# Performance work log

Hardware: AMD Instinct MI355X
Metric: run time of the kernel (lower is better)

Reference implementation:

```python
import jax, jax.numpy as jnp
import numpy as np
from jax import lax

PCR = (-59.9, -59.9, -2.0, 59.9, 59.9, 5.9)
TOPK = 10
THRESHOLD = 0.5
MARGIN = 0.5
EPS = 1e-8  # torch cosine_similarity default eps


def setup_inputs() -> dict:
    key = jax.random.key(0)
    k1, k2, k3, k4, k5 = jax.random.split(key, 5)
    B, C, H, W, N = 4, 64, 512, 512, 30
    loc_features = jax.random.normal(k1, (B, C, H, W), dtype=jnp.float32)
    det_features = jax.random.normal(k2, (B, C, H, W), dtype=jnp.float32)
    # gt boxes: x,y inside point-cloud range; last element is class id (0 == static)
    xy = jax.random.uniform(k3, (B, N, 2), minval=-55.0, maxval=55.0, dtype=jnp.float32)
    rest = jax.random.normal(k4, (B, N, 5), dtype=jnp.float32)
    cls = jax.random.randint(k5, (B, N, 1), 0, 3).astype(jnp.float32)
    gt_boxes = jnp.concatenate([xy, rest, cls], axis=-1)  # [B, N, 8]
    return {"loc_features": loc_features, "det_features": det_features, "gt_boxes": gt_boxes}


def _loss_fwd(loc_features, det_features, gt_boxes):
    B, C, H, W = loc_features.shape
    bw = PCR[3] - PCR[0]
    bh = PCR[4] - PCR[1]

    def per_batch(loc_fm, det_fm, boxes):
        # --- static GT detection features (gather at box centers) ---
        static_mask = boxes[:, -1] == 0  # [N]
        cx = jnp.clip(((boxes[:, 0] - PCR[0]) / bw * W).astype(jnp.int32), 0, W - 1)
        cy = jnp.clip(((boxes[:, 1] - PCR[1]) / bh * H).astype(jnp.int32), 0, H - 1)
        det_feats = det_fm[:, cy, cx].T  # [N, C]

        # --- find_peaks: local-max of L2 intensity, threshold, top-k (stop-grad) ---
        intensity = lax.stop_gradient(jnp.sqrt(jnp.sum(loc_fm * loc_fm, axis=0)))  # [H, W]
        pooled = lax.reduce_window(intensity, -jnp.inf, lax.max, (3, 3), (1, 1), [(1, 1), (1, 1)])
        peak_mask = (intensity == pooled) & (intensity > THRESHOLD)
        masked = jnp.where(peak_mask, intensity, -jnp.inf).reshape(-1)
        vals, idx = lax.top_k(masked, TOPK)  # descending by intensity
        valid_peak = jnp.isfinite(vals)  # handles < TOPK peaks
        py, px = idx // W, idx % W
        peak_feats = loc_fm[:, py, px].T  # [K, C]

        # --- pairwise cosine similarity (torch eps semantics) ---
        dn = det_feats / jnp.maximum(jnp.linalg.norm(det_feats, axis=-1, keepdims=True), EPS)
        pn = peak_feats / jnp.maximum(jnp.linalg.norm(peak_feats, axis=-1, keepdims=True), EPS)
        sim = jnp.einsum('nc,kc->nk', dn, pn)  # [N, K]

        pair_mask = (static_mask[:, None] & valid_peak[None, :]).astype(sim.dtype)
        n_pairs = jnp.sum(pair_mask)
        loss_sum = jnp.sum(jax.nn.relu(sim - MARGIN) * pair_mask)
        return jnp.where(n_pairs > 0, loss_sum / jnp.maximum(n_pairs, 1.0), 0.0)

    losses = jax.vmap(per_batch)(loc_features, det_features, gt_boxes)  # [B]
    return jnp.sum(losses) / B


def reference(loc_features, det_features, gt_boxes):
    return _loss_fwd(loc_features, det_features, gt_boxes)
```

## Files before the change

kernel.cpp:

```cpp
#include <hip/hip_runtime.h>
#include <math.h>

typedef unsigned long long u64;
typedef unsigned int u32;
typedef float f4 __attribute__((ext_vector_type(4)));

#define HH 512
#define WW 512
#define CC 64
#define HWHW (HH * WW)
#define NBOX 30
#define KTOP 10
#define BLKS_PER_B 256
#define CAND_PER_BATCH (BLKS_PER_B * KTOP)

__global__ void k_intensity(const float* __restrict__ loc, float* __restrict__ inten) {
    int t   = threadIdx.x;
    int blk = blockIdx.x;
    int b   = blk >> 7;
    int j   = blk & 127;
    const f4* base = reinterpret_cast<const f4*>(loc + (size_t)b * CC * HWHW);
    int q0 = j * 512 + t;
    int q1 = q0 + 256;

    f4 s0 = {0.f, 0.f, 0.f, 0.f};
    f4 s1 = {0.f, 0.f, 0.f, 0.f};
    #pragma unroll 8
    for (int c = 0; c < CC; ++c) {
        const f4* p = base + (size_t)c * (HWHW / 4);
        f4 v0 = __builtin_nontemporal_load(p + q0);
        f4 v1 = __builtin_nontemporal_load(p + q1);
        s0 += v0 * v0;
        s1 += v1 * v1;
    }
    f4 o0, o1;
    o0[0] = sqrtf(s0[0]); o0[1] = sqrtf(s0[1]); o0[2] = sqrtf(s0[2]); o0[3] = sqrtf(s0[3]);
    o1[0] = sqrtf(s1[0]); o1[1] = sqrtf(s1[1]); o1[2] = sqrtf(s1[2]); o1[3] = sqrtf(s1[3]);
    f4* out = reinterpret_cast<f4*>(inten + (size_t)b * HWHW);
    out[q0] = o0;
    out[q1] = o1;
}

__global__ void k_peakblock(const float* __restrict__ inten, u64* __restrict__ cand) {
    int t    = threadIdx.x;
    int lane = t & 63;
    int blk  = blockIdx.x;
    int b    = blk >> 8;
    int pblk = blk & 255;
    const float* I = inten + (size_t)b * HWHW;
    int pix0 = pblk * 1024 + t * 4;
    int y  = pix0 >> 9;
    int x0 = pix0 & (WW - 1);

    float w00,w01,w02,w03,w04,w05, w10,w11,w12,w13,w14,w15, w20,w21,w22,w23,w24,w25;
    {
        bool r0 = (y - 1) >= 0, r2 = (y + 1) < HH;
        bool c0 = (x0 - 1) >= 0, c5 = (x0 + 4) < WW;
        const float* Rm = I + (y - 1) * WW + x0;
        const float* Rc = I + y * WW + x0;
        const float* Rp = I + (y + 1) * WW + x0;
        w00 = (r0 && c0) ? Rm[-1] : -INFINITY;
        w01 = r0 ? Rm[0] : -INFINITY;  w02 = r0 ? Rm[1] : -INFINITY;
        w03 = r0 ? Rm[2] : -INFINITY;  w04 = r0 ? Rm[3] : -INFINITY;
        w05 = (r0 && c5) ? Rm[4] : -INFINITY;
        w10 = c0 ? Rc[-1] : -INFINITY;
        w11 = Rc[0]; w12 = Rc[1]; w13 = Rc[2]; w14 = Rc[3];
        w15 = c5 ? Rc[4] : -INFINITY;
        w20 = (r2 && c0) ? Rp[-1] : -INFINITY;
        w21 = r2 ? Rp[0] : -INFINITY;  w22 = r2 ? Rp[1] : -INFINITY;
        w23 = r2 ? Rp[2] : -INFINITY;  w24 = r2 ? Rp[3] : -INFINITY;
        w25 = (r2 && c5) ? Rp[4] : -INFINITY;
    }

    u64 k0, k1, k2, k3;
    {
        float m, v;
        v = w11;
        m = fmaxf(fmaxf(fmaxf(w00, w01), fmaxf(w02, w10)),
                  fmaxf(fmaxf(w11, w12), fmaxf(fmaxf(w20, w21), w22)));
        k0 = (v > 0.5f && v == m) ? (((u64)(__float_as_uint(v) | 0x80000000u) << 32) | (u32)(~(u32)(pix0 + 0))) : 0ull;
        v = w12;
        m = fmaxf(fmaxf(fmaxf(w01, w02), fmaxf(w03, w11)),
                  fmaxf(fmaxf(w12, w13), fmaxf(fmaxf(w21, w22), w23)));
        k1 = (v > 0.5f && v == m) ? (((u64)(__float_as_uint(v) | 0x80000000u) << 32) | (u32)(~(u32)(pix0 + 1))) : 0ull;
        v = w13;
        m = fmaxf(fmaxf(fmaxf(w02, w03), fmaxf(w04, w12)),
                  fmaxf(fmaxf(w13, w14), fmaxf(fmaxf(w22, w23), w24)));
        k2 = (v > 0.5f && v == m) ? (((u64)(__float_as_uint(v) | 0x80000000u) << 32) | (u32)(~(u32)(pix0 + 2))) : 0ull;
        v = w14;
        m = fmaxf(fmaxf(fmaxf(w03, w04), fmaxf(w05, w13)),
                  fmaxf(fmaxf(w14, w15), fmaxf(fmaxf(w23, w24), w25)));
        k3 = (v > 0.5f && v == m) ? (((u64)(__float_as_uint(v) | 0x80000000u) << 32) | (u32)(~(u32)(pix0 + 3))) : 0ull;
    }

    u64 a[4]; int n = 0;
    if (k0) a[n++] = k0;
    if (k1) a[n++] = k1;
    if (k2) a[n++] = k2;
    if (k3) a[n++] = k3;

    __shared__ int cnt;
    __shared__ u64 pool[1024];
    if (t == 0) cnt = 0;
    __syncthreads();

    int incl = n;
    #pragma unroll
    for (int s = 1; s < 64; s <<= 1) {
        int o = __shfl_up(incl, s, 64);
        if (lane >= s) incl += o;
    }
    int excl = incl - n;
    int wtot = __shfl(incl, 63, 64);
    int base = 0;
    if (lane == 0 && wtot > 0) base = atomicAdd(&cnt, wtot);
    base = __shfl(base, 0, 64);
    for (int i = 0; i < n; ++i) pool[base + excl + i] = a[i];
    __syncthreads();

    int total = cnt;
    if (t < 64) {
        u64 lv[KTOP];
        #pragma unroll
        for (int i = 0; i < KTOP; ++i) lv[i] = 0ull;
        for (int j = lane; j < total; j += 64) {
            u64 v = pool[j];
            if (v > lv[KTOP - 1]) {
                lv[KTOP - 1] = v;
                #pragma unroll
                for (int m = KTOP - 1; m > 0; --m)
                    if (lv[m] > lv[m - 1]) { u64 tm = lv[m]; lv[m] = lv[m - 1]; lv[m - 1] = tm; }
            }
        }
        u64 mine = 0;
        #pragma unroll
        for (int r = 0; r < KTOP; ++r) {
            u64 wv = lv[0];
            #pragma unroll
            for (int s = 1; s < 64; s <<= 1) {
                u64 o = __shfl_xor(wv, s, 64);
                wv = (o > wv) ? o : wv;
            }
            if (lane == r) mine = wv;
            if (lv[0] == wv && wv != 0ull) {
                #pragma unroll
                for (int m = 0; m < KTOP - 1; ++m) lv[m] = lv[m + 1];
                lv[KTOP - 1] = 0ull;
            }
        }
        if (lane < KTOP)
            cand[(size_t)b * CAND_PER_BATCH + pblk * KTOP + lane] = mine;
    }
}

__global__ void k_loss(const float* __restrict__ loc, const float* __restrict__ det,
                       const float* __restrict__ boxes,
                       const u64* __restrict__ cand,
                       float* __restrict__ bloss) {
    int b = blockIdx.x;
    int t = threadIdx.x;
    int lane = t & 63;

    u64 lv[KTOP];
    #pragma unroll
    for (int i = 0; i < KTOP; ++i) lv[i] = 0ull;
    const u64* C = cand + (size_t)b * CAND_PER_BATCH;
    #pragma unroll
    for (int w = 0; w < CAND_PER_BATCH / 256; ++w) {
        u64 v = C[t + w * 256];
        if (v > lv[KTOP - 1]) {
            lv[KTOP - 1] = v;
            #pragma unroll
            for (int m = KTOP - 1; m > 0; --m)
                if (lv[m] > lv[m - 1]) { u64 tm = lv[m]; lv[m] = lv[m - 1]; lv[m - 1] = tm; }
        }
    }

    __shared__ u64 sc[40];
    __shared__ u64 stopk[KTOP];
    u64 wmine = 0;
    #pragma unroll
    for (int r = 0; r < KTOP; ++r) {
        u64 wv = lv[0];
        #pragma unroll
        for (int s = 1; s < 64; s <<= 1) {
            u64 o = __shfl_xor(wv, s, 64);
            wv = (o > wv) ? o : wv;
        }
        if (lane == r) wmine = wv;
        if (lv[0] == wv && wv != 0ull) {
            #pragma unroll
            for (int m = 0; m < KTOP - 1; ++m) lv[m] = lv[m + 1];
            lv[KTOP - 1] = 0ull;
        }
    }
    if (lane < KTOP) sc[(t >> 6) * KTOP + lane] = wmine;
    __syncthreads();

    if (t < 64) {
        u64 v = (t < 40) ? sc[t] : 0ull;
        u64 fm = 0;
        #pragma unroll
        for (int r = 0; r < KTOP; ++r) {
            u64 wv = v;
            #pragma unroll
            for (int s = 1; s < 64; s <<= 1) {
                u64 o = __shfl_xor(wv, s, 64);
                wv = (o > wv) ? o : wv;
            }
            if (t == r) fm = wv;
            if (v == wv && wv != 0ull) v = 0ull;
        }
        if (t < KTOP) stopk[t] = fm;
    }
    __syncthreads();

    __shared__ int topi[KTOP], tvalid[KTOP];
    if (t < KTOP) {
        u64 kk = stopk[t];
        tvalid[t] = (kk != 0ull) ? 1 : 0;
        topi[t] = (int)((~(u32)kk) & (HWHW - 1));
    }

    __shared__ int s_cx[NBOX], s_cy[NBOX], s_static[NBOX];
    if (t < NBOX) {
        const float* bx = boxes + ((size_t)b * NBOX + t) * 8;
        float fx = (bx[0] + 59.9f) / 119.8f * 512.0f;
        float fy = (bx[1] + 59.9f) / 119.8f * 512.0f;
        int cx = (int)fx; int cy = (int)fy;
        cx = min(max(cx, 0), WW - 1);
        cy = min(max(cy, 0), HH - 1);
        s_cx[t] = cx; s_cy[t] = cy;
        s_static[t] = (bx[7] == 0.0f) ? 1 : 0;
    }
    __syncthreads();

    __shared__ float pf[KTOP][CC];
    __shared__ float df[NBOX][CC];
    #pragma unroll
    for (int w = 0; w < 3; ++w) {
        int e = t + w * 256;
        if (e < KTOP * CC) {
            int k = e >> 6, c = e & 63;
            int pix = tvalid[k] ? topi[k] : 0;
            pf[k][c] = loc[((size_t)b * CC + c) * HWHW + pix];
        }
    }
    #pragma unroll
    for (int w = 0; w < 8; ++w) {
        int e = t + w * 256;
        if (e < NBOX * CC) {
            int n = e >> 6, c = e & 63;
            int pix = s_cy[n] * WW + s_cx[n];
            df[n][c] = det[((size_t)b * CC + c) * HWHW + pix];
        }
    }
    __syncthreads();

    __shared__ float invn[NBOX + KTOP];
    if (t < NBOX + KTOP) {
        float s = 0.f;
        if (t < NBOX) {
            for (int c = 0; c < CC; ++c) s += df[t][c] * df[t][c];
        } else {
            int k = t - NBOX;
            for (int c = 0; c < CC; ++c) s += pf[k][c] * pf[k][c];
        }
        invn[t] = 1.0f / fmaxf(sqrtf(s), 1e-8f);
    }
    __syncthreads();
    for (int e = t; e < NBOX * CC; e += 256) { int n = e >> 6; df[n][e & 63] *= invn[n]; }
    for (int e = t; e < KTOP * CC; e += 256) { int k = e >> 6; pf[k][e & 63] *= invn[NBOX + k]; }
    __syncthreads();

    float lsum = 0.f, cntp = 0.f;
    for (int p = t; p < NBOX * KTOP; p += 256) {
        int n = p / KTOP, k = p - n * KTOP;
        float dot = 0.f;
        for (int c = 0; c < CC; ++c) dot += df[n][c] * pf[k][c];
        if (s_static[n] && tvalid[k]) {
            float r = dot - 0.5f;
            if (r > 0.f) lsum += r;
            cntp += 1.f;
        }
    }
    __shared__ float hv[256];
    __shared__ float hc[256];
    hv[t] = lsum; hc[t] = cntp;
    __syncthreads();
    for (int s = 128; s > 0; s >>= 1) {
        if (t < s) { hv[t] += hv[t + s]; hc[t] += hc[t + s]; }
        __syncthreads();
    }
    if (t == 0) {
        float np = hc[0];
        bloss[b] = (np > 0.f) ? hv[0] / fmaxf(np, 1.0f) : 0.f;
    }
}

__global__ void k_final(const float* __restrict__ bloss, float* __restrict__ out, int B) {
    float s = 0.f;
    for (int b = 0; b < B; ++b) s += bloss[b];
    out[0] = s / (float)B;
}

extern "C" void kernel_launch(void* const* d_in, const int* in_sizes, int n_in,
                              void* d_out, int out_size, void* d_ws, size_t ws_size,
                              hipStream_t stream) {
    const float* loc   = (const float*)d_in[0];
    const float* det   = (const float*)d_in[1];
    const float* boxes = (const float*)d_in[2];
    float* out = (float*)d_out;

    int B = in_sizes[0] / (CC * HWHW);

    float* inten = (float*)d_ws;
    u64*   cand  = (u64*)(inten + (size_t)B * HWHW);
    float* bloss = (float*)(cand + (size_t)B * CAND_PER_BATCH);

    dim3 blk(256);
    int g1 = B * 128;
    hipLaunchKernelGGL(k_intensity, dim3(g1), blk, 0, stream, loc, inten);
    hipLaunchKernelGGL(k_peakblock, dim3(B * BLKS_PER_B), blk, 0, stream, inten, cand);
    hipLaunchKernelGGL(k_loss, dim3(B), blk, 0, stream, loc, det, boxes, cand, bloss);
    hipLaunchKernelGGL(k_final, dim3(1), dim3(1), 0, stream, bloss, out, B);
}
```

Before: 73.59 us.

## Fuse peak detection, loss, and final reduction into one kernel with flag sync

Merges the peak-block, per-batch loss and final-sum kernels into one launch. The extra loss blocks gather and normalise detection features first, then spin on per-block release/acquire flags until that batch's candidates are ready. The last finishing block, found through an atomic counter, computes the mean. This removes two kernel launches and overlaps the det gather with peak finding, at the cost of spin-waiting blocks. Correctness depends on the loss blocks being scheduled alongside the producer blocks, which they are since they have the highest block indices and all producers get dispatched first.

After: 116.0 us. 1.58x slower.

```diff
diff --git a/kernel.cpp b/kernel.cpp
--- a/kernel.cpp
+++ b/kernel.cpp
@@ -11,14 +11,19 @@
 #define HWHW (HH * WW)
 #define NBOX 30
 #define KTOP 10
-#define BLKS_PER_B 256
-#define CAND_PER_BATCH (BLKS_PER_B * KTOP)
-
-__global__ void k_intensity(const float* __restrict__ loc, float* __restrict__ inten) {
+#define NBLK 256
+#define CPB (NBLK * KTOP)
+
+__global__ void k_intensity(const float* __restrict__ loc, float* __restrict__ inten,
+                            u32* __restrict__ flags, int* __restrict__ done, int B) {
     int t   = threadIdx.x;
     int blk = blockIdx.x;
-    int b   = blk >> 7;
-    int j   = blk & 127;
+    if (blk < B) {
+        flags[blk * NBLK + t] = 0;
+        if (blk == 0 && t == 0) *done = 0;
+    }
+    int b = blk >> 7;
+    int j = blk & 127;
     const f4* base = reinterpret_cast<const f4*>(loc + (size_t)b * CC * HWHW);
     int q0 = j * 512 + t;
     int q1 = q0 + 256;
@@ -41,90 +46,180 @@
     out[q1] = o1;
 }
 
-__global__ void k_peakblock(const float* __restrict__ inten, u64* __restrict__ cand) {
+__global__ void k_fused(const float* __restrict__ loc, const float* __restrict__ det,
+                        const float* __restrict__ boxes, const float* __restrict__ inten,
+                        u64* __restrict__ cand, u32* __restrict__ flags,
+                        int* __restrict__ done, float* __restrict__ bloss,
+                        float* __restrict__ out, int B) {
+    __shared__ u64 shl[1664];
     int t    = threadIdx.x;
     int lane = t & 63;
+    int wid  = t >> 6;
     int blk  = blockIdx.x;
-    int b    = blk >> 8;
-    int pblk = blk & 255;
-    const float* I = inten + (size_t)b * HWHW;
-    int pix0 = pblk * 1024 + t * 4;
-    int y  = pix0 >> 9;
-    int x0 = pix0 & (WW - 1);
-
-    float w00,w01,w02,w03,w04,w05, w10,w11,w12,w13,w14,w15, w20,w21,w22,w23,w24,w25;
-    {
-        bool r0 = (y - 1) >= 0, r2 = (y + 1) < HH;
-        bool c0 = (x0 - 1) >= 0, c5 = (x0 + 4) < WW;
-        const float* Rm = I + (y - 1) * WW + x0;
-        const float* Rc = I + y * WW + x0;
-        const float* Rp = I + (y + 1) * WW + x0;
-        w00 = (r0 && c0) ? Rm[-1] : -INFINITY;
-        w01 = r0 ? Rm[0] : -INFINITY;  w02 = r0 ? Rm[1] : -INFINITY;
-        w03 = r0 ? Rm[2] : -INFINITY;  w04 = r0 ? Rm[3] : -INFINITY;
-        w05 = (r0 && c5) ? Rm[4] : -INFINITY;
-        w10 = c0 ? Rc[-1] : -INFINITY;
-        w11 = Rc[0]; w12 = Rc[1]; w13 = Rc[2]; w14 = Rc[3];
-        w15 = c5 ? Rc[4] : -INFINITY;
-        w20 = (r2 && c0) ? Rp[-1] : -INFINITY;
-        w21 = r2 ? Rp[0] : -INFINITY;  w22 = r2 ? Rp[1] : -INFINITY;
-        w23 = r2 ? Rp[2] : -INFINITY;  w24 = r2 ? Rp[3] : -INFINITY;
-        w25 = (r2 && c5) ? Rp[4] : -INFINITY;
-    }
-
-    u64 k0, k1, k2, k3;
-    {
-        float m, v;
-        v = w11;
-        m = fmaxf(fmaxf(fmaxf(w00, w01), fmaxf(w02, w10)),
-                  fmaxf(fmaxf(w11, w12), fmaxf(fmaxf(w20, w21), w22)));
-        k0 = (v > 0.5f && v == m) ? (((u64)(__float_as_uint(v) | 0x80000000u) << 32) | (u32)(~(u32)(pix0 + 0))) : 0ull;
-        v = w12;
-        m = fmaxf(fmaxf(fmaxf(w01, w02), fmaxf(w03, w11)),
-                  fmaxf(fmaxf(w12, w13), fmaxf(fmaxf(w21, w22), w23)));
-        k1 = (v > 0.5f && v == m) ? (((u64)(__float_as_uint(v) | 0x80000000u) << 32) | (u32)(~(u32)(pix0 + 1))) : 0ull;
-        v = w13;
-        m = fmaxf(fmaxf(fmaxf(w02, w03), fmaxf(w04, w12)),
-                  fmaxf(fmaxf(w13, w14), fmaxf(fmaxf(w22, w23), w24)));
-        k2 = (v > 0.5f && v == m) ? (((u64)(__float_as_uint(v) | 0x80000000u) << 32) | (u32)(~(u32)(pix0 + 2))) : 0ull;
-        v = w14;
-        m = fmaxf(fmaxf(fmaxf(w03, w04), fmaxf(w05, w13)),
-                  fmaxf(fmaxf(w14, w15), fmaxf(fmaxf(w23, w24), w25)));
-        k3 = (v > 0.5f && v == m) ? (((u64)(__float_as_uint(v) | 0x80000000u) << 32) | (u32)(~(u32)(pix0 + 3))) : 0ull;
-    }
-
-    u64 a[4]; int n = 0;
-    if (k0) a[n++] = k0;
-    if (k1) a[n++] = k1;
-    if (k2) a[n++] = k2;
-    if (k3) a[n++] = k3;
-
-    __shared__ int cnt;
-    __shared__ u64 pool[1024];
-    if (t == 0) cnt = 0;
-    __syncthreads();
-
-    int incl = n;
-    #pragma unroll
-    for (int s = 1; s < 64; s <<= 1) {
-        int o = __shfl_up(incl, s, 64);
-        if (lane >= s) incl += o;
-    }
-    int excl = incl - n;
-    int wtot = __shfl(incl, 63, 64);
-    int base = 0;
-    if (lane == 0 && wtot > 0) base = atomicAdd(&cnt, wtot);
-    base = __shfl(base, 0, 64);
-    for (int i = 0; i < n; ++i) pool[base + excl + i] = a[i];
-    __syncthreads();
-
-    int total = cnt;
-    if (t < 64) {
+
+    if (blk < B * NBLK) {
+        int b    = blk >> 8;
+        int pblk = blk & 255;
+        const float* I = inten + (size_t)b * HWHW;
+        int pix0 = pblk * 1024 + t * 4;
+        int y  = pix0 >> 9;
+        int x0 = pix0 & (WW - 1);
+
+        float w00,w01,w02,w03,w04,w05, w10,w11,w12,w13,w14,w15, w20,w21,w22,w23,w24,w25;
+        {
+            bool r0 = (y - 1) >= 0, r2 = (y + 1) < HH;
+            bool c0 = (x0 - 1) >= 0, c5 = (x0 + 4) < WW;
+            const float* Rm = I + (y - 1) * WW + x0;
+            const float* Rc = I + y * WW + x0;
+            const float* Rp = I + (y + 1) * WW + x0;
+            w00 = (r0 && c0) ? Rm[-1] : -INFINITY;
+            w01 = r0 ? Rm[0] : -INFINITY;  w02 = r0 ? Rm[1] : -INFINITY;
+            w03 = r0 ? Rm[2] : -INFINITY;  w04 = r0 ? Rm[3] : -INFINITY;
+            w05 = (r0 && c5) ? Rm[4] : -INFINITY;
+            w10 = c0 ? Rc[-1] : -INFINITY;
+            w11 = Rc[0]; w12 = Rc[1]; w13 = Rc[2]; w14 = Rc[3];
+            w15 = c5 ? Rc[4] : -INFINITY;
+            w20 = (r2 && c0) ? Rp[-1] : -INFINITY;
+            w21 = r2 ? Rp[0] : -INFINITY;  w22 = r2 ? Rp[1] : -INFINITY;
+            w23 = r2 ? Rp[2] : -INFINITY;  w24 = r2 ? Rp[3] : -INFINITY;
+            w25 = (r2 && c5) ? Rp[4] : -INFINITY;
+        }
+
+        u64 k0, k1, k2, k3;
+        {
+            float m, v;
+            v = w11;
+            m = fmaxf(fmaxf(fmaxf(w00, w01), fmaxf(w02, w10)),
+                      fmaxf(fmaxf(w11, w12), fmaxf(fmaxf(w20, w21), w22)));
+            k0 = (v > 0.5f && v == m) ? (((u64)(__float_as_uint(v) | 0x80000000u) << 32) | (u32)(~(u32)(pix0 + 0))) : 0ull;
+            v = w12;
+            m = fmaxf(fmaxf(fmaxf(w01, w02), fmaxf(w03, w11)),
+                      fmaxf(fmaxf(w12, w13), fmaxf(fmaxf(w21, w22), w23)));
+            k1 = (v > 0.5f && v == m) ? (((u64)(__float_as_uint(v) | 0x80000000u) << 32) | (u32)(~(u32)(pix0 + 1))) : 0ull;
+            v = w13;
+            m = fmaxf(fmaxf(fmaxf(w02, w03), fmaxf(w04, w12)),
+                      fmaxf(fmaxf(w13, w14), fmaxf(fmaxf(w22, w23), w24)));
+            k2 = (v > 0.5f && v == m) ? (((u64)(__float_as_uint(v) | 0x80000000u) << 32) | (u32)(~(u32)(pix0 + 2))) : 0ull;
+            v = w14;
+            m = fmaxf(fmaxf(fmaxf(w03, w04), fmaxf(w05, w13)),
+                      fmaxf(fmaxf(w14, w15), fmaxf(fmaxf(w23, w24), w25)));
+            k3 = (v > 0.5f && v == m) ? (((u64)(__float_as_uint(v) | 0x80000000u) << 32) | (u32)(~(u32)(pix0 + 3))) : 0ull;
+        }
+
+        u64 a[4]; int n = 0;
+        if (k0) a[n++] = k0;
+        if (k1) a[n++] = k1;
+        if (k2) a[n++] = k2;
+        if (k3) a[n++] = k3;
+
+        __shared__ int cnt;
+        if (t == 0) cnt = 0;
+        __syncthreads();
+
+        int incl = n;
+        #pragma unroll
+        for (int s = 1; s < 64; s <<= 1) {
+            int o = __shfl_up(incl, s, 64);
+            if (lane >= s) incl += o;
+        }
+        int excl = incl - n;
+        int wtot = __shfl(incl, 63, 64);
+        int base = 0;
+        if (lane == 0 && wtot > 0) base = atomicAdd(&cnt, wtot);
+        base = __shfl(base, 0, 64);
+        for (int i = 0; i < n; ++i) shl[base + excl + i] = a[i];
+        __syncthreads();
+
+        int total = cnt;
+        if (t < 64) {
+            u64 lv[KTOP];
+            #pragma unroll
+            for (int i = 0; i < KTOP; ++i) lv[i] = 0ull;
+            for (int j = lane; j < total; j += 64) {
+                u64 v = shl[j];
+                if (v > lv[KTOP - 1]) {
+                    lv[KTOP - 1] = v;
+                    #pragma unroll
+                    for (int m = KTOP - 1; m > 0; --m)
+                        if (lv[m] > lv[m - 1]) { u64 tm = lv[m]; lv[m] = lv[m - 1]; lv[m - 1] = tm; }
+                }
+            }
+            u64 mine = 0;
+            #pragma unroll
+            for (int r = 0; r < KTOP; ++r) {
+                u64 wv = lv[0];
+                #pragma unroll
+                for (int s = 1; s < 64; s <<= 1) {
+                    u64 o = __shfl_xor(wv, s, 64);
+                    wv = (o > wv) ? o : wv;
+                }
+                if (lane == r) mine = wv;
+                if (lv[0] == wv && wv != 0ull) {
+                    #pragma unroll
+                    for (int m = 0; m < KTOP - 1; ++m) lv[m] = lv[m + 1];
+                    lv[KTOP - 1] = 0ull;
+                }
+            }
+            if (lane < KTOP)
+                cand[(size_t)b * CPB + pblk * KTOP + lane] = mine;
+            if (lane == 0) {
+                __threadfence();
+                __hip_atomic_store(&flags[b * NBLK + pblk], 1u,
+                                   __ATOMIC_RELEASE, __HIP_MEMORY_SCOPE_AGENT);
+            }
+        }
+    } else {
+        int b = blk - B * NBLK;
+        __shared__ int s_cx[NBOX], s_cy[NBOX], s_static[NBOX];
+        __shared__ float pf[KTOP][CC], df[NBOX][CC], invn[NBOX + KTOP];
+        __shared__ float hv[256], hc[256];
+        __shared__ u64 sc[40], stopk[KTOP];
+        __shared__ int topi[KTOP], tvalid[KTOP];
+
+        if (t < NBOX) {
+            const float* bx = boxes + ((size_t)b * NBOX + t) * 8;
+            float fx = (bx[0] + 59.9f) / 119.8f * 512.0f;
+            float fy = (bx[1] + 59.9f) / 119.8f * 512.0f;
+            int cx = (int)fx; int cy = (int)fy;
+            cx = min(max(cx, 0), WW - 1);
+            cy = min(max(cy, 0), HH - 1);
+            s_cx[t] = cx; s_cy[t] = cy;
+            s_static[t] = (bx[7] == 0.0f) ? 1 : 0;
+        }
+        __syncthreads();
+        #pragma unroll
+        for (int w = 0; w < 8; ++w) {
+            int e = t + w * 256;
+            if (e < NBOX * CC) {
+                int n = e >> 6, c = e & 63;
+                int pix = s_cy[n] * WW + s_cx[n];
+                df[n][c] = det[((size_t)b * CC + c) * HWHW + pix];
+            }
+        }
+        __syncthreads();
+        if (t < NBOX) {
+            float s = 0.f;
+            for (int c = 0; c < CC; ++c) s += df[t][c] * df[t][c];
+            invn[t] = 1.0f / fmaxf(sqrtf(s), 1e-8f);
+        }
+        __syncthreads();
+        for (int e = t; e < NBOX * CC; e += 256) { int n = e >> 6; df[n][e & 63] *= invn[n]; }
+
+        int rdy;
+        do {
+            u32 f = __hip_atomic_load(&flags[b * NBLK + t],
+                                      __ATOMIC_ACQUIRE, __HIP_MEMORY_SCOPE_AGENT);
+            rdy = (f != 0);
+        } while (!__syncthreads_and(rdy));
+        __threadfence();
+
         u64 lv[KTOP];
         #pragma unroll
         for (int i = 0; i < KTOP; ++i) lv[i] = 0ull;
-        for (int j = lane; j < total; j += 64) {
-            u64 v = pool[j];
+        const u64* C = cand + (size_t)b * CPB;
+        #pragma unroll
+        for (int w = 0; w < CPB / 256; ++w) {
+            u64 v = C[t + w * 256];
             if (v > lv[KTOP - 1]) {
                 lv[KTOP - 1] = v;
                 #pragma unroll
@@ -132,7 +227,8 @@
                     if (lv[m] > lv[m - 1]) { u64 tm = lv[m]; lv[m] = lv[m - 1]; lv[m - 1] = tm; }
             }
         }
-        u64 mine = 0;
+
+        u64 wmine = 0;
         #pragma unroll
         for (int r = 0; r < KTOP; ++r) {
             u64 wv = lv[0];
@@ -141,167 +237,90 @@
                 u64 o = __shfl_xor(wv, s, 64);
                 wv = (o > wv) ? o : wv;
             }
-            if (lane == r) mine = wv;
+            if (lane == r) wmine = wv;
             if (lv[0] == wv && wv != 0ull) {
                 #pragma unroll
                 for (int m = 0; m < KTOP - 1; ++m) lv[m] = lv[m + 1];
                 lv[KTOP - 1] = 0ull;
             }
         }
-        if (lane < KTOP)
-            cand[(size_t)b * CAND_PER_BATCH + pblk * KTOP + lane] = mine;
+        if (lane < KTOP) sc[wid * KTOP + lane] = wmine;
+        __syncthreads();
+
+        if (t < 64) {
+            u64 v = (t < 40) ? sc[t] : 0ull;
+            u64 fm = 0;
+            #pragma unroll
+            for (int r = 0; r < KTOP; ++r) {
+                u64 wv = v;
+                #pragma unroll
+                for (int s = 1; s < 64; s <<= 1) {
+                    u64 o = __shfl_xor(wv, s, 64);
+                    wv = (o > wv) ? o : wv;
+                }
+                if (t == r) fm = wv;
+                if (v == wv && wv != 0ull) v = 0ull;
+            }
+            if (t < KTOP) stopk[t] = fm;
+        }
+        __syncthreads();
+
+        if (t < KTOP) {
+            u64 kk = stopk[t];
+            tvalid[t] = (kk != 0ull) ? 1 : 0;
+            topi[t] = (int)((~(u32)kk) & (HWHW - 1));
+        }
+        __syncthreads();
+
+        #pragma unroll
+        for (int w = 0; w < 3; ++w) {
+            int e = t + w * 256;
+            if (e < KTOP * CC) {
+                int k = e >> 6, c = e & 63;
+                int pix = tvalid[k] ? topi[k] : 0;
+                pf[k][c] = loc[((size_t)b * CC + c) * HWHW + pix];
+            }
+        }
+        __syncthreads();
+        if (t < KTOP) {
+            float s = 0.f;
+            for (int c = 0; c < CC; ++c) s += pf[t][c] * pf[t][c];
+            invn[NBOX + t] = 1.0f / fmaxf(sqrtf(s), 1e-8f);
+        }
+        __syncthreads();
+        for (int e = t; e < KTOP * CC; e += 256) { int k = e >> 6; pf[k][e & 63] *= invn[NBOX + k]; }
+        __syncthreads();
+
+        float lsum = 0.f, cntp = 0.f;
+        for (int p = t; p < NBOX * KTOP; p += 256) {
+            int n = p / KTOP, k = p - n * KTOP;
+            float dot = 0.f;
+            for (int c = 0; c < CC; ++c) dot += df[n][c] * pf[k][c];
+            if (s_static[n] && tvalid[k]) {
+                float r = dot - 0.5f;
+                if (r > 0.f) lsum += r;
+                cntp += 1.f;
+            }
+        }
+        hv[t] = lsum; hc[t] = cntp;
+        __syncthreads();
+        for (int s = 128; s > 0; s >>= 1) {
+            if (t < s) { hv[t] += hv[t + s]; hc[t] += hc[t + s]; }
+            __syncthreads();
+        }
+        if (t == 0) {
+            float np = hc[0];
+            bloss[b] = (np > 0.f) ? hv[0] / fmaxf(np, 1.0f) : 0.f;
+            __threadfence();
+            int old = atomicAdd(done, 1);
+            if (old == B - 1) {
+                __threadfence();
+                float s = 0.f;
+                for (int i = 0; i < B; ++i) s += bloss[i];
+                out[0] = s / (float)B;
+            }
+        }
     }
-}
-
-__global__ void k_loss(const float* __restrict__ loc, const float* __restrict__ det,
-                       const float* __restrict__ boxes,
-                       const u64* __restrict__ cand,
-                       float* __restrict__ bloss) {
-    int b = blockIdx.x;
-    int t = threadIdx.x;
-    int lane = t & 63;
-
-    u64 lv[KTOP];
-    #pragma unroll
-    for (int i = 0; i < KTOP; ++i) lv[i] = 0ull;
-    const u64* C = cand + (size_t)b * CAND_PER_BATCH;
-    #pragma unroll
-    for (int w = 0; w < CAND_PER_BATCH / 256; ++w) {
-        u64 v = C[t + w * 256];
-        if (v > lv[KTOP - 1]) {
-            lv[KTOP - 1] = v;
-            #pragma unroll
-            for (int m = KTOP - 1; m > 0; --m)
-                if (lv[m] > lv[m - 1]) { u64 tm = lv[m]; lv[m] = lv[m - 1]; lv[m - 1] = tm; }
-        }
-    }
-
-    __shared__ u64 sc[40];
-    __shared__ u64 stopk[KTOP];
-    u64 wmine = 0;
-    #pragma unroll
-    for (int r = 0; r < KTOP; ++r) {
-        u64 wv = lv[0];
-        #pragma unroll
-        for (int s = 1; s < 64; s <<= 1) {
-            u64 o = __shfl_xor(wv, s, 64);
-            wv = (o > wv) ? o : wv;
-        }
-        if (lane == r) wmine = wv;
-        if (lv[0] == wv && wv != 0ull) {
-            #pragma unroll
-            for (int m = 0; m < KTOP - 1; ++m) lv[m] = lv[m + 1];
-            lv[KTOP - 1] = 0ull;
-        }
-    }
-    if (lane < KTOP) sc[(t >> 6) * KTOP + lane] = wmine;
-    __syncthreads();
-
-    if (t < 64) {
-        u64 v = (t < 40) ? sc[t] : 0ull;
-        u64 fm = 0;
-        #pragma unroll
-        for (int r = 0; r < KTOP; ++r) {
-            u64 wv = v;
-            #pragma unroll
-            for (int s = 1; s < 64; s <<= 1) {
-                u64 o = __shfl_xor(wv, s, 64);
-                wv = (o > wv) ? o : wv;
-            }
-            if (t == r) fm = wv;
-            if (v == wv && wv != 0ull) v = 0ull;
-        }
-        if (t < KTOP) stopk[t] = fm;
-    }
-    __syncthreads();
-
-    __shared__ int topi[KTOP], tvalid[KTOP];
-    if (t < KTOP) {
-        u64 kk = stopk[t];
-        tvalid[t] = (kk != 0ull) ? 1 : 0;
-        topi[t] = (int)((~(u32)kk) & (HWHW - 1));
-    }
-
-    __shared__ int s_cx[NBOX], s_cy[NBOX], s_static[NBOX];
-    if (t < NBOX) {
-        const float* bx = boxes + ((size_t)b * NBOX + t) * 8;
-        float fx = (bx[0] + 59.9f) / 119.8f * 512.0f;
-        float fy = (bx[1] + 59.9f) / 119.8f * 512.0f;
-        int cx = (int)fx; int cy = (int)fy;
-        cx = min(max(cx, 0), WW - 1);
-        cy = min(max(cy, 0), HH - 1);
-        s_cx[t] = cx; s_cy[t] = cy;
-        s_static[t] = (bx[7] == 0.0f) ? 1 : 0;
-    }
-    __syncthreads();
-
-    __shared__ float pf[KTOP][CC];
-    __shared__ float df[NBOX][CC];
-    #pragma unroll
-    for (int w = 0; w < 3; ++w) {
-        int e = t + w * 256;
-        if (e < KTOP * CC) {
-            int k = e >> 6, c = e & 63;
-            int pix = tvalid[k] ? topi[k] : 0;
-            pf[k][c] = loc[((size_t)b * CC + c) * HWHW + pix];
-        }
-    }
-    #pragma unroll
-    for (int w = 0; w < 8; ++w) {
-        int e = t + w * 256;
-        if (e < NBOX * CC) {
-            int n = e >> 6, c = e & 63;
-            int pix = s_cy[n] * WW + s_cx[n];
-            df[n][c] = det[((size_t)b * CC + c) * HWHW + pix];
-        }
-    }
-    __syncthreads();
-
-    __shared__ float invn[NBOX + KTOP];
-    if (t < NBOX + KTOP) {
-        float s = 0.f;
-        if (t < NBOX) {
-            for (int c = 0; c < CC; ++c) s += df[t][c] * df[t][c];
-        } else {
-            int k = t - NBOX;
-            for (int c = 0; c < CC; ++c) s += pf[k][c] * pf[k][c];
-        }
-        invn[t] = 1.0f / fmaxf(sqrtf(s), 1e-8f);
-    }
-    __syncthreads();
-    for (int e = t; e < NBOX * CC; e += 256) { int n = e >> 6; df[n][e & 63] *= invn[n]; }
-    for (int e = t; e < KTOP * CC; e += 256) { int k = e >> 6; pf[k][e & 63] *= invn[NBOX + k]; }
-    __syncthreads();
-
-    float lsum = 0.f, cntp = 0.f;
-    for (int p = t; p < NBOX * KTOP; p += 256) {
-        int n = p / KTOP, k = p - n * KTOP;
-        float dot = 0.f;
-        for (int c = 0; c < CC; ++c) dot += df[n][c] * pf[k][c];
-        if (s_static[n] && tvalid[k]) {
-            float r = dot - 0.5f;
-            if (r > 0.f) lsum += r;
-            cntp += 1.f;
-        }
-    }
-    __shared__ float hv[256];
-    __shared__ float hc[256];
-    hv[t] = lsum; hc[t] = cntp;
-    __syncthreads();
-    for (int s = 128; s > 0; s >>= 1) {
-        if (t < s) { hv[t] += hv[t + s]; hc[t] += hc[t + s]; }
-        __syncthreads();
-    }
-    if (t == 0) {
-        float np = hc[0];
-        bloss[b] = (np > 0.f) ? hv[0] / fmaxf(np, 1.0f) : 0.f;
-    }
-}
-
-__global__ void k_final(const float* __restrict__ bloss, float* __restrict__ out, int B) {
-    float s = 0.f;
-    for (int b = 0; b < B; ++b) s += bloss[b];
-    out[0] = s / (float)B;
 }
 
 extern "C" void kernel_launch(void* const* d_in, const int* in_sizes, int n_in,
@@ -316,12 +335,12 @@
 
     float* inten = (float*)d_ws;
     u64*   cand  = (u64*)(inten + (size_t)B * HWHW);
-    float* bloss = (float*)(cand + (size_t)B * CAND_PER_BATCH);
+    u32*   flags = (u32*)(cand + (size_t)B * CPB);
+    int*   done  = (int*)(flags + (size_t)B * NBLK);
+    float* bloss = (float*)(done + 2);
 
     dim3 blk(256);
-    int g1 = B * 128;
-    hipLaunchKernelGGL(k_intensity, dim3(g1), blk, 0, stream, loc, inten);
-    hipLaunchKernelGGL(k_peakblock, dim3(B * BLKS_PER_B), blk, 0, stream, inten, cand);
-    hipLaunchKernelGGL(k_loss, dim3(B), blk, 0, stream, loc, det, boxes, cand, bloss);
-    hipLaunchKernelGGL(k_final, dim3(1), dim3(1), 0, stream, bloss, out, B);
+    hipLaunchKernelGGL(k_intensity, dim3(B * 128), blk, 0, stream, loc, inten, flags, done, B);
+    hipLaunchKernelGGL(k_fused, dim3(B * NBLK + B), blk, 0, stream,
+                       loc, det, boxes, inten, cand, flags, done, bloss, out, B);
 }
```
